# Kernel tuning notes

Hardware: AMD Instinct MI355X
Metric: run time of the kernel (lower is better)

## Reference

```python
import jax, jax.numpy as jnp
import numpy as np

B, S, H = 2, 2048, 2048
N_HEADS = 16
HEAD_DIM = H // N_HEADS  # 128


def apply_rotary(x, cos, sin):
    # x: (B, n_heads, S, head_dim); cos/sin: (S, head_dim//2)
    d = x.shape[-1] // 2
    x1, x2 = x[..., :d], x[..., d:]
    c = cos[None, None, :x.shape[2]]
    s = sin[None, None, :x.shape[2]]
    return jnp.concatenate([x1 * c - x2 * s, x2 * c + x1 * s], axis=-1)


def setup_inputs() -> dict:
    key = jax.random.key(0)
    k1, k2, k3 = jax.random.split(key, 3)
    x = jax.random.normal(k1, (B, S, H), dtype=jnp.float32)
    qkv_w = jax.random.normal(k2, (3 * H, H), dtype=jnp.float32) * (1.0 / np.sqrt(H))
    o_w = jax.random.normal(k3, (H, H), dtype=jnp.float32) * (1.0 / np.sqrt(H))
    # rotary tables, half head_dim
    inv_freq = 1.0 / (10000.0 ** (jnp.arange(0, HEAD_DIM // 2, dtype=jnp.float32) / (HEAD_DIM // 2)))
    t = jnp.arange(S, dtype=jnp.float32)
    freqs = jnp.outer(t, inv_freq)  # (S, head_dim//2)
    cos, sin = jnp.cos(freqs), jnp.sin(freqs)
    # True = masked (strictly upper triangular)
    causal_mask = jnp.triu(jnp.ones((S, S), dtype=bool), k=1)
    return {"x": x, "qkv_w": qkv_w, "o_w": o_w, "cos": cos, "sin": sin,
            "causal_mask": causal_mask}


def reference(x, qkv_w, o_w, cos, sin, causal_mask):
    Bx, Sx, Hx = x.shape
    qkv = jnp.einsum('bsh,oh->bso', x, qkv_w)  # (B,S,3H)
    qkv = qkv.reshape(Bx, Sx, 3, N_HEADS, HEAD_DIM)
    q, k, v = qkv[:, :, 0], qkv[:, :, 1], qkv[:, :, 2]
    q = jnp.transpose(q, (0, 2, 1, 3))  # (B,nh,S,hd)
    k = jnp.transpose(k, (0, 2, 1, 3))
    v = jnp.transpose(v, (0, 2, 1, 3))
    q = apply_rotary(q, cos, sin)
    k = apply_rotary(k, cos, sin)
    scale = 1.0 / jnp.sqrt(jnp.asarray(HEAD_DIM, dtype=x.dtype))
    attn = jnp.einsum('bnqd,bnkd->bnqk', q, k) * scale
    attn = jnp.where(causal_mask[None, None], -jnp.inf, attn)
    attn = jax.nn.softmax(attn, axis=-1)
    out = jnp.einsum('bnqk,bnkd->bnqd', attn, v)
    out = jnp.transpose(out, (0, 2, 1, 3)).reshape(Bx, Sx, Hx)
    return jnp.einsum('bsh,oh->bso', out, o_w)
```

## Files before the change

kernel.cpp:

```cpp
#include <hip/hip_runtime.h>
#include <hip/hip_bf16.h>
#include <stdint.h>

typedef __attribute__((ext_vector_type(4))) float f32x4;
typedef __attribute__((ext_vector_type(8))) short s16x8;
typedef __attribute__((ext_vector_type(4))) short s16x4;

#define SWZ(g, row) ((((g) & ~7) | (((g) ^ ((row) & 7)) & 7)))

__device__ __forceinline__ unsigned short f2bf(float f) {
  unsigned u = __builtin_bit_cast(unsigned, f);
  u += 0x7fffu + ((u >> 16) & 1u);
  return (unsigned short)(u >> 16);
}

__device__ __forceinline__ void gld16(const void* g, void* l) {
  __builtin_amdgcn_global_load_lds(
      (const __attribute__((address_space(1))) void*)g,
      (__attribute__((address_space(3))) void*)l, 16, 0, 0);
}

__global__ void cvt_all(const float* __restrict__ x, const float* __restrict__ qkvw,
                        const float* __restrict__ ow, unsigned short* __restrict__ X16,
                        unsigned short* __restrict__ W16, unsigned short* __restrict__ OW16) {
  int i = blockIdx.x * blockDim.x + threadIdx.x;
  const float* src; unsigned short* dst; int off;
  if (i < 2097152)      { src = x;    dst = X16;  off = i; }
  else if (i < 5242880) { src = qkvw; dst = W16;  off = i - 2097152; }
  else                  { src = ow;   dst = OW16; off = i - 5242880; }
  float4 v = ((const float4*)src)[off];
  s16x4 o;
  o[0] = (short)f2bf(v.x); o[1] = (short)f2bf(v.y);
  o[2] = (short)f2bf(v.z); o[3] = (short)f2bf(v.w);
  ((s16x4*)dst)[off] = o;
}

#define STAGE384(BB, KT) \
  { char* dA = smem + (BB) * 65536; \
    char* dB = dA + 16384; \
    _Pragma("unroll") for (int rr = 0; rr < 2; ++rr) { \
      const int G = rr * 512 + tid; const int row = G >> 3, g = G & 7; \
      gld16((const char*)(Aorg + (size_t)row * 2048 + (size_t)(KT) * 64) + (SWZ(g, row) << 4), \
            dA + rr * 8192 + tid * 16); } \
    _Pragma("unroll") for (int rr = 0; rr < 6; ++rr) { \
      const int G = rr * 512 + tid; const int row = G >> 3, g = G & 7; \
      gld16((const char*)(Borg + (size_t)row * 2048 + (size_t)(KT) * 64) + (SWZ(g, row) << 4), \
            dB + rr * 8192 + tid * 16); } }

#define RDA(KS) \
  _Pragma("unroll") for (int j = 0; j < 4; ++j) { \
    const int ra = wm * 64 + j * 16 + lg; \
    av[j] = *(const s16x8*)(sA + ra * 128 + (SWZ(4 * (KS) + hg, ra) << 4)); }

#define RDB(KS, CH) \
  _Pragma("unroll") for (int b = 0; b < 3; ++b) { \
    const int bb = (CH) * 3 + b; \
    const int cb = (bb >> 1) * 128 + wn * 16 + (bb & 1) * 64 + lg; \
    bv[b] = *(const s16x8*)(sB + cb * 128 + (SWZ(4 * (KS) + hg, cb) << 4)); }

#define MM12(CH) \
  _Pragma("unroll") for (int j = 0; j < 4; ++j) \
    _Pragma("unroll") for (int b = 0; b < 3; ++b) \
      acc[j][(CH) * 3 + b] = __builtin_amdgcn_mfma_f32_16x16x32_bf16( \
          av[j], bv[b], acc[j][(CH) * 3 + b], 0, 0, 0);

#define PH_PRE \
  __builtin_amdgcn_s_barrier(); \
  asm volatile("s_waitcnt lgkmcnt(0)" ::: "memory"); \
  __builtin_amdgcn_sched_barrier(0); \
  __builtin_amdgcn_s_setprio(1);

#define PH_POST \
  __builtin_amdgcn_s_setprio(0); \
  __builtin_amdgcn_s_barrier();

__global__ __launch_bounds__(512, 1) void gemm_qkv_384(
    const unsigned short* __restrict__ A,
    const unsigned short* __restrict__ Bt,
    const float* __restrict__ cosT, const float* __restrict__ sinT,
    unsigned short* __restrict__ qOut, unsigned short* __restrict__ kOut,
    unsigned short* __restrict__ vtOut)
{
  __shared__ char smem[131072];
  const int tid = (int)threadIdx.x;
  const int wid = tid >> 6, l = tid & 63;
  const int lg = l & 15, hg = l >> 4;
  const int wm = wid >> 2, wn = wid & 3;
  const int s = ((int)blockIdx.x & 7) * 64 + ((int)blockIdx.x >> 3);
  const int bm0 = (s & 31) * 128, bn0 = (s >> 5) * 384;

  const unsigned short* Aorg = A + (size_t)bm0 * 2048;
  const unsigned short* Borg = Bt + (size_t)bn0 * 2048;

  f32x4 acc[4][6] = {};

  STAGE384(0, 0)
  for (int t = 0; t < 31; ++t) {
    STAGE384((t & 1) ^ 1, t + 1)
    asm volatile("s_waitcnt vmcnt(8)" ::: "memory");
    __builtin_amdgcn_s_barrier();
    const char* sA = smem + (t & 1) * 65536;
    const char* sB = sA + 16384;
    s16x8 av[4], bv[3];
    RDA(0) RDB(0, 0)  PH_PRE  MM12(0)  PH_POST
    RDB(0, 1)         PH_PRE  MM12(1)  PH_POST
    RDA(1) RDB(1, 1)  PH_PRE  MM12(1)  PH_POST
    RDB(1, 0)         PH_PRE  MM12(0)  PH_POST
  }
  {
    asm volatile("s_waitcnt vmcnt(0)" ::: "memory");
    __builtin_amdgcn_s_barrier();
    const char* sA = smem + 65536;
    const char* sB = sA + 16384;
    s16x8 av[4], bv[3];
    RDA(0) RDB(0, 0)  PH_PRE  MM12(0)  PH_POST
    RDB(0, 1)         PH_PRE  MM12(1)  PH_POST
    RDA(1) RDB(1, 1)  PH_PRE  MM12(1)  PH_POST
    RDB(1, 0)         PH_PRE  MM12(0)  PH_POST
  }

  #pragma unroll
  for (int j = 0; j < 4; ++j) {
    const int grow0 = bm0 + wm * 64 + j * 16 + hg * 4;
    const int b_ = grow0 >> 11;
    #pragma unroll
    for (int cg = 0; cg < 3; ++cg) {
      const int og = (bn0 >> 7) + cg;
      const int tt = og >> 4, h = og & 15;
      const int d = wn * 16 + lg;
      if (tt < 2) {
        unsigned short* dst = (tt == 0) ? qOut : kOut;
        #pragma unroll
        for (int r = 0; r < 4; ++r) {
          const int gr = grow0 + r;
          const int s1 = gr & 2047;
          const float x1 = acc[j][cg * 2 + 0][r];
          const float x2 = acc[j][cg * 2 + 1][r];
          const float cv = cosT[s1 * 64 + d];
          const float sv = sinT[s1 * 64 + d];
          const size_t base = (((size_t)b_ * 16 + h) * 2048 + s1) * 128;
          dst[base + d]      = f2bf(x1 * cv - x2 * sv);
          dst[base + d + 64] = f2bf(x2 * cv + x1 * sv);
        }
      } else {
        const int s0 = grow0 & 2047;
        s16x4 p1, p2;
        #pragma unroll
        for (int r = 0; r < 4; ++r) {
          p1[r] = (short)f2bf(acc[j][cg * 2 + 0][r]);
          p2[r] = (short)f2bf(acc[j][cg * 2 + 1][r]);
        }
        *(s16x4*)(vtOut + (((size_t)b_ * 16 + h) * 128 + d)      * 2048 + s0) = p1;
        *(s16x4*)(vtOut + (((size_t)b_ * 16 + h) * 128 + d + 64) * 2048 + s0) = p2;
      }
    }
  }
}

#define STAGEOP(BB, KT) \
  { char* dA = smem + (BB) * 49152; \
    char* dB = dA + 16384; \
    _Pragma("unroll") for (int rr = 0; rr < 2; ++rr) { \
      const int G = rr * 512 + tid; const int row = G >> 3, g = G & 7; \
      gld16((const char*)(Aorg + (size_t)row * 2048 + (size_t)(KT) * 64) + (SWZ(g, row) << 4), \
            dA + rr * 8192 + tid * 16); } \
    _Pragma("unroll") for (int rr = 0; rr < 4; ++rr) { \
      const int G = rr * 512 + tid; const int row = G >> 3, g = G & 7; \
      gld16((const char*)(Borg + (size_t)row * 2048 + (size_t)(KT) * 64) + (SWZ(g, row) << 4), \
            dB + rr * 8192 + tid * 16); } }

#define RDBO(KS, CH) \
  _Pragma("unroll") for (int b = 0; b < 2; ++b) { \
    const int cb = ((CH) * 2 + b) * 64 + wn * 16 + lg; \
    bv[b] = *(const s16x8*)(sB + cb * 128 + (SWZ(4 * (KS) + hg, cb) << 4)); }

#define MMO(CH) \
  _Pragma("unroll") for (int j = 0; j < 4; ++j) \
    _Pragma("unroll") for (int b = 0; b < 2; ++b) \
      acc[j][(CH) * 2 + b] = __builtin_amdgcn_mfma_f32_16x16x32_bf16( \
          av[j], bv[b], acc[j][(CH) * 2 + b], 0, 0, 0);

__global__ __launch_bounds__(512, 1) void gemm_op_256(
    const unsigned short* __restrict__ A,
    const unsigned short* __restrict__ Bt,
    float* __restrict__ C)
{
  __shared__ char smem[98304];
  const int tid = (int)threadIdx.x;
  const int wid = tid >> 6, l = tid & 63;
  const int lg = l & 15, hg = l >> 4;
  const int wm = wid >> 2, wn = wid & 3;
  const int s = ((int)blockIdx.x & 7) * 32 + ((int)blockIdx.x >> 3);
  const int bm0 = (s & 31) * 128, bn0 = (s >> 5) * 256;

  const unsigned short* Aorg = A + (size_t)bm0 * 2048;
  const unsigned short* Borg = Bt + (size_t)bn0 * 2048;

  f32x4 acc[4][4] = {};

  STAGEOP(0, 0)
  for (int t = 0; t < 31; ++t) {
    STAGEOP((t & 1) ^ 1, t + 1)
    asm volatile("s_waitcnt vmcnt(6)" ::: "memory");
    __builtin_amdgcn_s_barrier();
    const char* sA = smem + (t & 1) * 49152;
    const char* sB = sA + 16384;
    s16x8 av[4], bv[2];
    RDA(0) RDBO(0, 0)  PH_PRE  MMO(0)  PH_POST
    RDBO(0, 1)         PH_PRE  MMO(1)  PH_POST
    RDA(1) RDBO(1, 1)  PH_PRE  MMO(1)  PH_POST
    RDBO(1, 0)         PH_PRE  MMO(0)  PH_POST
  }
  {
    asm volatile("s_waitcnt vmcnt(0)" ::: "memory");
    __builtin_amdgcn_s_barrier();
    const char* sA = smem + 49152;
    const char* sB = sA + 16384;
    s16x8 av[4], bv[2];
    RDA(0) RDBO(0, 0)  PH_PRE  MMO(0)  PH_POST
    RDBO(0, 1)         PH_PRE  MMO(1)  PH_POST
    RDA(1) RDBO(1, 1)  PH_PRE  MMO(1)  PH_POST
    RDBO(1, 0)         PH_PRE  MMO(0)  PH_POST
  }

  #pragma unroll
  for (int j = 0; j < 4; ++j) {
    const int row0 = bm0 + wm * 64 + j * 16 + hg * 4;
    #pragma unroll
    for (int b = 0; b < 4; ++b) {
      const int col = bn0 + b * 64 + wn * 16 + lg;
      #pragma unroll
      for (int r = 0; r < 4; ++r)
        C[(size_t)(row0 + r) * 2048 + col] = acc[j][b][r];
    }
  }
}

__global__ __launch_bounds__(256) void attn_fwd(
    const unsigned short* __restrict__ Qp, const unsigned short* __restrict__ Kp,
    const unsigned short* __restrict__ Vt, unsigned short* __restrict__ AO)
{
  __shared__ char sK[16384];
  __shared__ char sV[16384];
  __shared__ char sP[8192];

  const int tid = (int)threadIdx.x, w = tid >> 6, l = tid & 63;
  const int lg = l & 15, hg = l >> 4;
  const int bid = (int)blockIdx.x;
  const int p = bid >> 8, c = bid & 255;
  const int j = c >> 5, bh = c & 31;
  const int qt = (p == 0) ? j : (p == 1) ? 31 - j : (p == 2) ? 8 + j : 23 - j;
  const size_t qkBase = (size_t)bh * 2048 * 128;
  const int qw0 = qt * 64 + w * 16;
  const int qi = qw0 + lg;

  s16x8 qf[4];
  for (int ks = 0; ks < 4; ++ks)
    qf[ks] = *(const s16x8*)(Qp + qkBase + (size_t)(qw0 + lg) * 128 + ks * 32 + hg * 8);

  f32x4 acc_o[8] = {};
  float mrun = -1e30f, lrun = 0.f;
  const float SCALE = 0.08838834764831845f;
  const float L2E = 1.4426950408889634f;
  const float CS = SCALE * L2E;

  const int nkv = qt + 1;
  for (int kv = 0; kv < nkv; ++kv) {
    const int kv0 = kv * 64;
    __syncthreads();
    for (int i = 0; i < 4; ++i) {
      const int G = w * 256 + i * 64 + l;
      const int rk = G >> 4, gk = G & 15;
      gld16((const char*)(Kp + qkBase + (size_t)(kv0 + rk) * 128) + (SWZ(gk, rk) << 4),
            sK + w * 4096 + i * 1024);
      const int rv = G >> 3, gv = G & 7;
      gld16((const char*)(Vt + qkBase + (size_t)rv * 2048 + kv0) + (SWZ(gv, rv) << 4),
            sV + w * 4096 + i * 1024);
    }
    asm volatile("s_waitcnt vmcnt(0)" ::: "memory");
    __syncthreads();

    f32x4 accs[4] = {};
    for (int ks = 0; ks < 4; ++ks)
      for (int kf = 0; kf < 4; ++kf) {
        const int row = kf * 16 + lg;
        const int g = SWZ(4 * ks + hg, row);
        s16x8 kfrag = *(const s16x8*)(sK + row * 256 + (g << 4));
        accs[kf] = __builtin_amdgcn_mfma_f32_16x16x32_bf16(kfrag, qf[ks], accs[kf], 0, 0, 0);
      }

    const bool diag = (kv == qt);
    float raw[4][4];
    float mt = -1e30f;
    #pragma unroll
    for (int kf = 0; kf < 4; ++kf)
      #pragma unroll
      for (int r = 0; r < 4; ++r) {
        float s = accs[kf][r];
        if (diag) {
          const int jj = kv0 + kf * 16 + hg * 4 + r;
          s = (jj > qi) ? -1e30f : s;
        }
        raw[kf][r] = s;
        mt = fmaxf(mt, s);
      }
    mt = fmaxf(mt, __shfl_xor(mt, 16));
    mt = fmaxf(mt, __shfl_xor(mt, 32));
    mt *= SCALE;
    if (!__all(mt - mrun <= 8.0f)) {
      const float mnew = fmaxf(mrun, mt);
      const float alpha = exp2f((mrun - mnew) * L2E);
      float ar[4];
      #pragma unroll
      for (int r = 0; r < 4; ++r) ar[r] = __shfl(alpha, hg * 4 + r);
      #pragma unroll
      for (int f = 0; f < 8; ++f)
        #pragma unroll
        for (int r = 0; r < 4; ++r) acc_o[f][r] *= ar[r];
      lrun *= alpha;
      mrun = mnew;
    }
    const float mL = mrun * L2E;
    float ls = 0.f;
    char* pw = sP + w * 2048;
    #pragma unroll
    for (int kf = 0; kf < 4; ++kf) {
      s16x4 pk;
      #pragma unroll
      for (int r = 0; r < 4; ++r) {
        const float e = exp2f(raw[kf][r] * CS - mL);
        ls += e;
        pk[r] = (short)f2bf(e);
      }
      const int j0 = kf * 16 + hg * 4;
      *(s16x4*)(pw + lg * 128 + (SWZ(j0 >> 3, lg) << 4) + ((j0 * 2) & 15)) = pk;
    }
    ls += __shfl_xor(ls, 16);
    ls += __shfl_xor(ls, 32);
    lrun += ls;
    asm volatile("" ::: "memory");

    for (int jc = 0; jc < 2; ++jc) {
      const int gp = SWZ(hg + 4 * jc, lg);
      s16x8 pa = *(const s16x8*)(pw + lg * 128 + (gp << 4));
      for (int f = 0; f < 8; ++f) {
        const int rv = f * 16 + lg;
        const int gv = SWZ(hg + 4 * jc, rv);
        s16x8 vb = *(const s16x8*)(sV + rv * 128 + (gv << 4));
        acc_o[f] = __builtin_amdgcn_mfma_f32_16x16x32_bf16(pa, vb, acc_o[f], 0, 0, 0);
      }
    }
  }

  float linv[4];
  for (int r = 0; r < 4; ++r) linv[r] = 1.0f / __shfl(lrun, hg * 4 + r);
  const int b = bh >> 4, h = bh & 15;
  for (int f = 0; f < 8; ++f) {
    const int d = h * 128 + f * 16 + lg;
    for (int r = 0; r < 4; ++r) {
      const int srow = qw0 + hg * 4 + r;
      AO[((size_t)(b * 2048 + srow)) * 2048 + d] = f2bf(acc_o[f][r] * linv[r]);
    }
  }
}

extern "C" void kernel_launch(void* const* d_in, const int* in_sizes, int n_in,
                              void* d_out, int out_size, void* d_ws, size_t ws_size,
                              hipStream_t stream) {
  const float* x    = (const float*)d_in[0];
  const float* qkvw = (const float*)d_in[1];
  const float* ow   = (const float*)d_in[2];
  const float* cosT = (const float*)d_in[3];
  const float* sinT = (const float*)d_in[4];
  float* out = (float*)d_out;

  unsigned short* X16  = (unsigned short*)d_ws;
  unsigned short* W16  = X16  + (size_t)8388608;
  unsigned short* OW16 = W16  + (size_t)12582912;
  unsigned short* Qp   = OW16 + (size_t)4194304;
  unsigned short* Kp   = Qp   + (size_t)8388608;
  unsigned short* Vtp  = Kp   + (size_t)8388608;
  unsigned short* AO   = Vtp  + (size_t)8388608;

  cvt_all<<<24576, 256, 0, stream>>>(x, qkvw, ow, X16, W16, OW16);

  gemm_qkv_384<<<512, 512, 0, stream>>>(X16, W16, cosT, sinT, Qp, Kp, Vtp);

  attn_fwd<<<1024, 256, 0, stream>>>(Qp, Kp, Vtp, AO);

  gemm_op_256<<<256, 512, 0, stream>>>(AO, OW16, out);
}
```

Before: 253.0 us.

## Interleave next-tile global-to-LDS loads across MFMA phases in both GEMMs

Splits the per-iteration staging of the next K tile into chunks issued between the four MFMA phases, replacing one bulk issue at the top of the loop. The vmcnt waits are moved to the phase boundaries so that only the chunk about to be consumed must have landed. This spreads memory traffic across the compute and shortens the stall at the iteration boundary. In exchange, the wait counts must exactly match the in-flight loads per thread, which adds fragility, and issuing loads inside the phases may contend with LDS reads.

```diff
diff --git a/kernel.cpp b/kernel.cpp
--- a/kernel.cpp
+++ b/kernel.cpp
@@ -35,22 +35,47 @@
   ((s16x4*)dst)[off] = o;
 }
 
-#define STAGE384(BB, KT) \
-  { char* dA = smem + (BB) * 65536; \
-    char* dB = dA + 16384; \
-    _Pragma("unroll") for (int rr = 0; rr < 2; ++rr) { \
-      const int G = rr * 512 + tid; const int row = G >> 3, g = G & 7; \
-      gld16((const char*)(Aorg + (size_t)row * 2048 + (size_t)(KT) * 64) + (SWZ(g, row) << 4), \
-            dA + rr * 8192 + tid * 16); } \
-    _Pragma("unroll") for (int rr = 0; rr < 6; ++rr) { \
-      const int G = rr * 512 + tid; const int row = G >> 3, g = G & 7; \
-      gld16((const char*)(Borg + (size_t)row * 2048 + (size_t)(KT) * 64) + (SWZ(g, row) << 4), \
-            dB + rr * 8192 + tid * 16); } }
+#define PH_PRE \
+  __builtin_amdgcn_s_barrier(); \
+  asm volatile("s_waitcnt lgkmcnt(0)" ::: "memory"); \
+  __builtin_amdgcn_sched_barrier(0); \
+  __builtin_amdgcn_s_setprio(1);
+
+#define PH_POST_N \
+  __builtin_amdgcn_s_setprio(0); \
+  __builtin_amdgcn_s_barrier();
+
+#define PH_POST_W0 \
+  __builtin_amdgcn_s_setprio(0); \
+  asm volatile("s_waitcnt vmcnt(0)" ::: "memory"); \
+  __builtin_amdgcn_s_barrier();
+
+#define PH_POST_W2 \
+  __builtin_amdgcn_s_setprio(0); \
+  asm volatile("s_waitcnt vmcnt(2)" ::: "memory"); \
+  __builtin_amdgcn_s_barrier();
+
+#define PH_POST_W3 \
+  __builtin_amdgcn_s_setprio(0); \
+  asm volatile("s_waitcnt vmcnt(3)" ::: "memory"); \
+  __builtin_amdgcn_s_barrier();
 
 #define RDA(KS) \
   _Pragma("unroll") for (int j = 0; j < 4; ++j) { \
     const int ra = wm * 64 + j * 16 + lg; \
     av[j] = *(const s16x8*)(sA + ra * 128 + (SWZ(4 * (KS) + hg, ra) << 4)); }
+
+#define STG_A(DST, ORG, KT) \
+  _Pragma("unroll") for (int rr = 0; rr < 2; ++rr) { \
+    const int G = rr * 512 + tid; const int row = G >> 3, g = G & 7; \
+    gld16((const char*)((ORG) + (size_t)row * 2048 + (size_t)(KT) * 64) + (SWZ(g, row) << 4), \
+          (DST) + rr * 8192 + tid * 16); }
+
+#define STG_B2(DST, ORG, KT, R0) \
+  _Pragma("unroll") for (int rr = (R0); rr < (R0) + 2; ++rr) { \
+    const int G = rr * 512 + tid; const int row = G >> 3, g = G & 7; \
+    gld16((const char*)((ORG) + (size_t)row * 2048 + (size_t)(KT) * 64) + (SWZ(g, row) << 4), \
+          (DST) + rr * 8192 + tid * 16); }
 
 #define RDB(KS, CH) \
   _Pragma("unroll") for (int b = 0; b < 3; ++b) { \
@@ -63,16 +88,6 @@
     _Pragma("unroll") for (int b = 0; b < 3; ++b) \
       acc[j][(CH) * 3 + b] = __builtin_amdgcn_mfma_f32_16x16x32_bf16( \
           av[j], bv[b], acc[j][(CH) * 3 + b], 0, 0, 0);
-
-#define PH_PRE \
-  __builtin_amdgcn_s_barrier(); \
-  asm volatile("s_waitcnt lgkmcnt(0)" ::: "memory"); \
-  __builtin_amdgcn_sched_barrier(0); \
-  __builtin_amdgcn_s_setprio(1);
-
-#define PH_POST \
-  __builtin_amdgcn_s_setprio(0); \
-  __builtin_amdgcn_s_barrier();
 
 __global__ __launch_bounds__(512, 1) void gemm_qkv_384(
     const unsigned short* __restrict__ A,
@@ -94,29 +109,33 @@
 
   f32x4 acc[4][6] = {};
 
-  STAGE384(0, 0)
+  STG_A(smem + 0, Aorg, 0)
+  STG_B2(smem + 16384, Borg, 0, 0)
+  STG_B2(smem + 16384, Borg, 0, 2)
+  STG_B2(smem + 16384, Borg, 0, 4)
+  asm volatile("s_waitcnt vmcnt(3)" ::: "memory");
+  __builtin_amdgcn_s_barrier();
+
   for (int t = 0; t < 31; ++t) {
-    STAGE384((t & 1) ^ 1, t + 1)
-    asm volatile("s_waitcnt vmcnt(8)" ::: "memory");
-    __builtin_amdgcn_s_barrier();
     const char* sA = smem + (t & 1) * 65536;
     const char* sB = sA + 16384;
+    char* dA = smem + ((t & 1) ^ 1) * 65536;
+    char* dB = dA + 16384;
     s16x8 av[4], bv[3];
-    RDA(0) RDB(0, 0)  PH_PRE  MM12(0)  PH_POST
-    RDB(0, 1)         PH_PRE  MM12(1)  PH_POST
-    RDA(1) RDB(1, 1)  PH_PRE  MM12(1)  PH_POST
-    RDB(1, 0)         PH_PRE  MM12(0)  PH_POST
+    RDA(0) RDB(0, 0) STG_A(dA, Aorg, t + 1)      PH_PRE MM12(0) PH_POST_W2
+    RDB(0, 1)        STG_B2(dB, Borg, t + 1, 0)  PH_PRE MM12(1) PH_POST_N
+    RDA(1) RDB(1, 1) STG_B2(dB, Borg, t + 1, 2)  PH_PRE MM12(1) PH_POST_N
+    RDB(1, 0)        STG_B2(dB, Borg, t + 1, 4)  PH_PRE MM12(0) PH_POST_W3
   }
   {
-    asm volatile("s_waitcnt vmcnt(0)" ::: "memory");
-    __builtin_amdgcn_s_barrier();
     const char* sA = smem + 65536;
     const char* sB = sA + 16384;
     s16x8 av[4], bv[3];
-    RDA(0) RDB(0, 0)  PH_PRE  MM12(0)  PH_POST
-    RDB(0, 1)         PH_PRE  MM12(1)  PH_POST
-    RDA(1) RDB(1, 1)  PH_PRE  MM12(1)  PH_POST
-    RDB(1, 0)         PH_PRE  MM12(0)  PH_POST
+    RDA(0) RDB(0, 0)  PH_PRE MM12(0) PH_POST_W0
+    RDB(0, 1)         PH_PRE MM12(1) PH_POST_N
+    RDA(1) RDB(1, 1)  PH_PRE MM12(1) PH_POST_N
+    RDB(1, 0)         PH_PRE MM12(0)
+    __builtin_amdgcn_s_setprio(0);
   }
 
   #pragma unroll
@@ -157,18 +176,6 @@
   }
 }
 
-#define STAGEOP(BB, KT) \
-  { char* dA = smem + (BB) * 49152; \
-    char* dB = dA + 16384; \
-    _Pragma("unroll") for (int rr = 0; rr < 2; ++rr) { \
-      const int G = rr * 512 + tid; const int row = G >> 3, g = G & 7; \
-      gld16((const char*)(Aorg + (size_t)row * 2048 + (size_t)(KT) * 64) + (SWZ(g, row) << 4), \
-            dA + rr * 8192 + tid * 16); } \
-    _Pragma("unroll") for (int rr = 0; rr < 4; ++rr) { \
-      const int G = rr * 512 + tid; const int row = G >> 3, g = G & 7; \
-      gld16((const char*)(Borg + (size_t)row * 2048 + (size_t)(KT) * 64) + (SWZ(g, row) << 4), \
-            dB + rr * 8192 + tid * 16); } }
-
 #define RDBO(KS, CH) \
   _Pragma("unroll") for (int b = 0; b < 2; ++b) { \
     const int cb = ((CH) * 2 + b) * 64 + wn * 16 + lg; \
@@ -198,29 +205,32 @@
 
   f32x4 acc[4][4] = {};
 
-  STAGEOP(0, 0)
+  STG_A(smem + 0, Aorg, 0)
+  STG_B2(smem + 16384, Borg, 0, 0)
+  STG_B2(smem + 16384, Borg, 0, 2)
+  asm volatile("s_waitcnt vmcnt(2)" ::: "memory");
+  __builtin_amdgcn_s_barrier();
+
   for (int t = 0; t < 31; ++t) {
-    STAGEOP((t & 1) ^ 1, t + 1)
-    asm volatile("s_waitcnt vmcnt(6)" ::: "memory");
-    __builtin_amdgcn_s_barrier();
     const char* sA = smem + (t & 1) * 49152;
     const char* sB = sA + 16384;
+    char* dA = smem + ((t & 1) ^ 1) * 49152;
+    char* dB = dA + 16384;
     s16x8 av[4], bv[2];
-    RDA(0) RDBO(0, 0)  PH_PRE  MMO(0)  PH_POST
-    RDBO(0, 1)         PH_PRE  MMO(1)  PH_POST
-    RDA(1) RDBO(1, 1)  PH_PRE  MMO(1)  PH_POST
-    RDBO(1, 0)         PH_PRE  MMO(0)  PH_POST
+    RDA(0) RDBO(0, 0) STG_A(dA, Aorg, t + 1)      PH_PRE MMO(0) PH_POST_W2
+    RDBO(0, 1)        STG_B2(dB, Borg, t + 1, 0)  PH_PRE MMO(1) PH_POST_N
+    RDA(1) RDBO(1, 1) STG_B2(dB, Borg, t + 1, 2)  PH_PRE MMO(1) PH_POST_N
+    RDBO(1, 0)                                    PH_PRE MMO(0) PH_POST_W2
   }
   {
-    asm volatile("s_waitcnt vmcnt(0)" ::: "memory");
-    __builtin_amdgcn_s_barrier();
     const char* sA = smem + 49152;
     const char* sB = sA + 16384;
     s16x8 av[4], bv[2];
-    RDA(0) RDBO(0, 0)  PH_PRE  MMO(0)  PH_POST
-    RDBO(0, 1)         PH_PRE  MMO(1)  PH_POST
-    RDA(1) RDBO(1, 1)  PH_PRE  MMO(1)  PH_POST
-    RDBO(1, 0)         PH_PRE  MMO(0)  PH_POST
+    RDA(0) RDBO(0, 0)  PH_PRE MMO(0) PH_POST_W0
+    RDBO(0, 1)         PH_PRE MMO(1) PH_POST_N
+    RDA(1) RDBO(1, 1)  PH_PRE MMO(1) PH_POST_N
+    RDBO(1, 0)         PH_PRE MMO(0)
+    __builtin_amdgcn_s_setprio(0);
   }
 
   #pragma unroll
```

Result: faster. 234.1 us, median of 3 (-7.4%).
